# Performance work log

Measured on AMD Instinct MI355X. Metric: run time of the kernel, lower is better.

Reference implementation:

```python
import jax, jax.numpy as jnp
import numpy as np

EPS = 1e-5  # BatchNorm eps (torch default)

def setup_inputs() -> dict:
    key = jax.random.key(0)
    ks = jax.random.split(key, 24)
    B, NX, NY, F = 8, 128, 128, 128
    dims = [2 * F, 512, 256, 128, 64]
    d = {
        'x': jax.random.normal(ks[0], (B, NX, F), dtype=jnp.float32),
        'y': jax.random.normal(ks[1], (B, NY, F), dtype=jnp.float32),
    }
    i = 2
    for li, (din, dout) in enumerate(zip(dims[:-1], dims[1:]), start=1):
        d[f'w{li}'] = jax.random.normal(ks[i], (dout, din), dtype=jnp.float32) * (1.0 / np.sqrt(din)); i += 1
        d[f'b{li}'] = jax.random.normal(ks[i], (dout,), dtype=jnp.float32) * 0.02; i += 1
        if li < 4:  # BatchNorm1d on hidden layers only (eval mode: running stats)
            d[f'g{li}'] = 1.0 + 0.1 * jax.random.normal(ks[i], (dout,), dtype=jnp.float32); i += 1
            d[f'be{li}'] = 0.1 * jax.random.normal(ks[i], (dout,), dtype=jnp.float32); i += 1
            d[f'm{li}'] = 0.1 * jax.random.normal(ks[i], (dout,), dtype=jnp.float32); i += 1
            d[f'v{li}'] = 0.5 + jax.random.uniform(ks[i], (dout,), dtype=jnp.float32); i += 1
    return d

def _bn(h, g, be, m, v):
    # BatchNorm1d in eval mode over the channel (last) axis
    return (h - m) * (g * jax.lax.rsqrt(v + EPS)) + be

def reference(x, y,
              w1, b1, g1, be1, m1, v1,
              w2, b2, g2, be2, m2, v2,
              w3, b3, g3, be3, m3, v3,
              w4, b4):
    F = x.shape[-1]
    # First Linear on cat([x_i, y_j]) == split-weight broadcast add: avoids the
    # (B,nx,ny,2F) pairwise concat the torch code materializes (same math).
    wx, wy = w1[:, :F], w1[:, F:]                      # (512,F) each
    hx = jnp.einsum('bif,hf->bih', x, wx)              # (B,nx,512)
    hy = jnp.einsum('bjf,hf->bjh', y, wy)              # (B,ny,512)
    h = hx[:, :, None, :] + hy[:, None, :, :] + b1     # (B,nx,ny,512)
    h = jax.nn.relu(_bn(h, g1, be1, m1, v1))           # dropout is identity in eval
    h = jax.nn.relu(_bn(jnp.einsum('bijh,oh->bijo', h, w2) + b2, g2, be2, m2, v2))
    h = jax.nn.relu(_bn(jnp.einsum('bijh,oh->bijo', h, w3) + b3, g3, be3, m3, v3))
    e = jnp.einsum('bijh,oh->bijo', h, w4) + b4        # (B,nx,ny,64) embeddings
    # PSD path: einsum('bijk,bilk->bijl', e, e).sum(-1)
    #         == sum_k e[b,i,j,k] * (sum_l e[b,i,l,k])  -- avoids (B,nx,ny,ny)
    s = e.sum(axis=2)                                  # (B,nx,64)
    kernel = jnp.einsum('bijk,bik->bij', e, s)         # (B,nx,ny)
    return kernel
```

## Files before the change

### kernel.cpp

```cpp
#include <hip/hip_runtime.h>

#define EPS 1e-5f

typedef _Float16 half8 __attribute__((ext_vector_type(8)));
typedef _Float16 half4 __attribute__((ext_vector_type(4)));
typedef float f32x16 __attribute__((ext_vector_type(16)));
typedef float f32x4v __attribute__((ext_vector_type(4)));


__global__ __launch_bounds__(256)
void pre_kernel(
    const float* __restrict__ x, const float* __restrict__ y,
    const float* __restrict__ w1, const float* __restrict__ b1,
    const float* __restrict__ g1, const float* __restrict__ be1,
    const float* __restrict__ m1, const float* __restrict__ v1,
    const float* __restrict__ w2, const float* __restrict__ b2,
    const float* __restrict__ g2, const float* __restrict__ be2,
    const float* __restrict__ m2, const float* __restrict__ v2,
    const float* __restrict__ w3, const float* __restrict__ b3,
    const float* __restrict__ g3, const float* __restrict__ be3,
    const float* __restrict__ m3, const float* __restrict__ v3,
    const float* __restrict__ w4,
    _Float16* __restrict__ hxh, _Float16* __restrict__ hyh,
    _Float16* __restrict__ w2h, _Float16* __restrict__ w3h,
    _Float16* __restrict__ w4h,
    float* __restrict__ b2f, float* __restrict__ b3f)
{
    const int t = threadIdx.x;

    if (blockIdx.x >= 256) {
        int tid = (blockIdx.x - 256) * 256 + t;
        const int nth = 64 * 256;
        for (int idx = tid; idx < 256 * 512; idx += nth) {
            int n = idx >> 9, k = idx & 511;
            float a = g2[n] * rsqrtf(v2[n] + EPS);
            int addr = ((n >> 5) * 32 + (k >> 4)) * 512 + ((k >> 3) & 1) * 256 + (n & 31) * 8 + (k & 7);
            w2h[addr] = (_Float16)(a * w2[idx]);
        }
        for (int idx = tid; idx < 128 * 256; idx += nth) {
            int n = idx >> 8, k = idx & 255;
            float a = g3[n] * rsqrtf(v3[n] + EPS);
            int addr = ((n >> 5) * 16 + (k >> 4)) * 512 + ((k >> 3) & 1) * 256 + (n & 31) * 8 + (k & 7);
            w3h[addr] = (_Float16)(a * w3[idx]);
        }
        for (int idx = tid; idx < 64 * 128; idx += nth) {
            int n = idx >> 7, k = idx & 127;
            int addr = ((n >> 5) * 8 + (k >> 4)) * 512 + ((k >> 3) & 1) * 256 + (n & 31) * 8 + (k & 7);
            w4h[addr] = (_Float16)w4[idx];
        }
        if (tid < 256) {
            float a = g2[tid] * rsqrtf(v2[tid] + EPS);
            b2f[tid] = a * b2[tid] + be2[tid] - m2[tid] * a;
        } else if (tid < 384) {
            int n = tid - 256;
            float a = g3[n] * rsqrtf(v3[n] + EPS);
            b3f[n] = a * b3[n] + be3[n] - m3[n] * a;
        }
        return;
    }

    const int rg = blockIdx.x & 31;
    const int ng = (blockIdx.x >> 5) & 3;
    const int which = blockIdx.x >> 7;

    constexpr int LDA = 136;
    __shared__ _Float16 sh[32 * 136 + 128 * 136] __attribute__((aligned(16)));
    _Float16* xa = sh;
    _Float16* wb = sh + 32 * 136;

    const int rowbase = rg * 32;
    const float* src = which ? y : x;

#pragma unroll
    for (int p = 0; p < 4; ++p) {
        int c = p * 256 + t;
        int r = c >> 5, fo = (c & 31) * 4;
        f32x4v v = *(const f32x4v*)(src + (size_t)(rowbase + r) * 128 + fo);
        half4 h; h[0] = (_Float16)v[0]; h[1] = (_Float16)v[1];
        h[2] = (_Float16)v[2]; h[3] = (_Float16)v[3];
        *(half4*)(xa + r * LDA + fo) = h;
    }
#pragma unroll
    for (int p = 0; p < 16; ++p) {
        int c = p * 256 + t;
        int n = c >> 5, fo = (c & 31) * 4;
        f32x4v v = *(const f32x4v*)(w1 + (size_t)(ng * 128 + n) * 256 + which * 128 + fo);
        half4 h; h[0] = (_Float16)v[0]; h[1] = (_Float16)v[1];
        h[2] = (_Float16)v[2]; h[3] = (_Float16)v[3];
        *(half4*)(wb + n * LDA + fo) = h;
    }
    __syncthreads();

    const int wid = t >> 6;
    const int l = t & 63;
    const int l31 = l & 31, lh = l >> 5;

    f32x16 acc = (f32x16)0.f;
#pragma unroll
    for (int kc = 0; kc < 8; ++kc) {
        half8 af = *(const half8*)(xa + l31 * LDA + kc * 16 + lh * 8);
        half8 bf = *(const half8*)(wb + (wid * 32 + l31) * LDA + kc * 16 + lh * 8);
        acc = __builtin_amdgcn_mfma_f32_32x32x16_f16(af, bf, acc, 0, 0, 0);
    }

    const int n = ng * 128 + wid * 32 + l31;
    float alpha = g1[n] * rsqrtf(v1[n] + EPS);
    if (which == 0) {
        float bias = alpha * b1[n] + be1[n] - m1[n] * alpha;
#pragma unroll
        for (int r = 0; r < 16; ++r) {
            int m = (r & 3) + 8 * (r >> 2) + 4 * lh;
            hxh[(size_t)(rowbase + m) * 512 + n] = (_Float16)(alpha * acc[r] + bias);
        }
    } else {
        const int ks = n >> 4, lhh = (n >> 3) & 1, c = n & 7;
#pragma unroll
        for (int r = 0; r < 16; ++r) {
            int m = (r & 3) + 8 * (r >> 2) + 4 * lh;
            int R = rowbase + m;
            int bb = R >> 7, j = R & 127;
            int addr = bb * 65536 + ((j >> 5) * 32 + ks) * 512 + lhh * 256 + (j & 31) * 8 + c;
            hyh[addr] = (_Float16)(alpha * acc[r]);
        }
    }
}

__global__ __launch_bounds__(512, 2)
void fused_kernel(
    const _Float16* __restrict__ hxh, const _Float16* __restrict__ hyh,
    const _Float16* __restrict__ w2h, const _Float16* __restrict__ w3h,
    const _Float16* __restrict__ w4h,
    const float* __restrict__ b2f, const float* __restrict__ b3f,
    const float* __restrict__ b4,
    float* __restrict__ out)
{
    constexpr int LD2 = 264;
    constexpr int LD3 = 136;
    constexpr int LDE = 68;

    __shared__ char smem[4352 + 67584] __attribute__((aligned(16)));
    _Float16* hxs = (_Float16*)smem;
    float* spart  = (float*)(smem + 2048);
    float* ss     = (float*)(smem + 4096);
    char* R1 = smem + 4352;
    _Float16* a2  = (_Float16*)R1;
    _Float16* a3  = (_Float16*)R1;
    float*    es  = (float*)R1;

    const int b  = blockIdx.x >> 6;
    const int ip = blockIdx.x & 63;
    const int i0 = ip * 2;
    const int t = threadIdx.x;
    const int wid = t >> 6;
    const int l   = t & 63;
    const int l31 = l & 31;
    const int lh  = l >> 5;

    if (t < 128) {
        int iv = t >> 6;
        *(half8*)(hxs + iv * 512 + (t & 63) * 8) =
            *(const half8*)(hxh + (size_t)(b * 128 + i0 + iv) * 512 + (t & 63) * 8);
    }
    __syncthreads();

    const int wm = wid >> 2, wn = wid & 3;

    const _Float16* pa0 = hyh + (size_t)b * 65536 + (size_t)(2 * wm) * 32 * 512 + l * 8;
    const _Float16* pa1 = pa0 + 32 * 512;
    const _Float16* pb0 = w2h + (size_t)(2 * wn) * 32 * 512 + l * 8;
    const _Float16* pb1 = pb0 + 32 * 512;

    const float bb0 = b2f[wn * 64 + l31];
    const float bb1 = b2f[wn * 64 + 32 + l31];
    f32x16 d00 = (f32x16)bb0, d01 = (f32x16)bb1;
    f32x16 d10 = (f32x16)bb0, d11 = (f32x16)bb1;
    f32x16 e00 = (f32x16)bb0, e01 = (f32x16)bb1;
    f32x16 e10 = (f32x16)bb0, e11 = (f32x16)bb1;

    half8 A00, A01, B00, B01;
    half8 A10, A11, B10, B11;

    auto LD0 = [&](int ks) {
        A00 = *(const half8*)(pa0 + (size_t)ks * 512);
        A01 = *(const half8*)(pa1 + (size_t)ks * 512);
        B00 = *(const half8*)(pb0 + (size_t)ks * 512);
        B01 = *(const half8*)(pb1 + (size_t)ks * 512);
    };
    auto LD1 = [&](int ks) {
        A10 = *(const half8*)(pa0 + (size_t)ks * 512);
        A11 = *(const half8*)(pa1 + (size_t)ks * 512);
        B10 = *(const half8*)(pb0 + (size_t)ks * 512);
        B11 = *(const half8*)(pb1 + (size_t)ks * 512);
    };
    auto RELU = [&](half8 a, half8 rx) {
        half8 s = a + rx;
        half8 af;
#pragma unroll
        for (int c = 0; c < 8; ++c)
            af[c] = s[c] > (_Float16)0.f ? s[c] : (_Float16)0.f;
        return af;
    };
    auto STEP0 = [&](int ks) {
        half8 rx0 = *(const half8*)(hxs + ks * 16 + lh * 8);
        half8 rx1 = *(const half8*)(hxs + 512 + ks * 16 + lh * 8);
        half8 af;
        af = RELU(A00, rx0);
        d00 = __builtin_amdgcn_mfma_f32_32x32x16_f16(af, B00, d00, 0, 0, 0);
        d01 = __builtin_amdgcn_mfma_f32_32x32x16_f16(af, B01, d01, 0, 0, 0);
        af = RELU(A01, rx0);
        d10 = __builtin_amdgcn_mfma_f32_32x32x16_f16(af, B00, d10, 0, 0, 0);
        d11 = __builtin_amdgcn_mfma_f32_32x32x16_f16(af, B01, d11, 0, 0, 0);
        af = RELU(A00, rx1);
        e00 = __builtin_amdgcn_mfma_f32_32x32x16_f16(af, B00, e00, 0, 0, 0);
        e01 = __builtin_amdgcn_mfma_f32_32x32x16_f16(af, B01, e01, 0, 0, 0);
        af = RELU(A01, rx1);
        e10 = __builtin_amdgcn_mfma_f32_32x32x16_f16(af, B00, e10, 0, 0, 0);
        e11 = __builtin_amdgcn_mfma_f32_32x32x16_f16(af, B01, e11, 0, 0, 0);
    };
    auto STEP1 = [&](int ks) {
        half8 rx0 = *(const half8*)(hxs + ks * 16 + lh * 8);
        half8 rx1 = *(const half8*)(hxs + 512 + ks * 16 + lh * 8);
        half8 af;
        af = RELU(A10, rx0);
        d00 = __builtin_amdgcn_mfma_f32_32x32x16_f16(af, B10, d00, 0, 0, 0);
        d01 = __builtin_amdgcn_mfma_f32_32x32x16_f16(af, B11, d01, 0, 0, 0);
        af = RELU(A11, rx0);
        d10 = __builtin_amdgcn_mfma_f32_32x32x16_f16(af, B10, d10, 0, 0, 0);
        d11 = __builtin_amdgcn_mfma_f32_32x32x16_f16(af, B11, d11, 0, 0, 0);
        af = RELU(A10, rx1);
        e00 = __builtin_amdgcn_mfma_f32_32x32x16_f16(af, B10, e00, 0, 0, 0);
        e01 = __builtin_amdgcn_mfma_f32_32x32x16_f16(af, B11, e01, 0, 0, 0);
        af = RELU(A11, rx1);
        e10 = __builtin_amdgcn_mfma_f32_32x32x16_f16(af, B10, e10, 0, 0, 0);
        e11 = __builtin_amdgcn_mfma_f32_32x32x16_f16(af, B11, e11, 0, 0, 0);
    };

    LD0(0);
#pragma unroll 2
    for (int ks = 0; ks < 32; ks += 2) {
        if (ks + 1 < 32) LD1(ks + 1);
        STEP0(ks);
        if (ks + 2 < 32) LD0(ks + 2);
        if (ks + 1 < 32) STEP1(ks + 1);
    }

    auto TAIL = [&](const f32x16& a00, const f32x16& a01,
                    const f32x16& a10, const f32x16& a11, int iv) {
#pragma unroll
        for (int r = 0; r < 16; ++r) {
            int m = wm * 64 + (r & 3) + 8 * (r >> 2) + 4 * lh;
            a2[m * LD2 + wn * 64 + l31]               = (_Float16)fmaxf(a00[r], 0.f);
            a2[m * LD2 + wn * 64 + 32 + l31]          = (_Float16)fmaxf(a01[r], 0.f);
            a2[(m + 32) * LD2 + wn * 64 + l31]        = (_Float16)fmaxf(a10[r], 0.f);
            a2[(m + 32) * LD2 + wn * 64 + 32 + l31]   = (_Float16)fmaxf(a11[r], 0.f);
        }
        __syncthreads();

        f32x16 g0, g1;
        {
            float b3v = b3f[wn * 32 + l31];
            g0 = (f32x16)b3v;
            g1 = (f32x16)b3v;
        }
#pragma unroll 4
        for (int kc = 0; kc < 16; ++kc) {
            half8 bfr = *(const half8*)(w3h + (wn * 16 + kc) * 512 + l * 8);
            half8 af0 = *(const half8*)(a2 + (wm * 64 + l31) * LD2 + kc * 16 + lh * 8);
            half8 af1 = *(const half8*)(a2 + (wm * 64 + 32 + l31) * LD2 + kc * 16 + lh * 8);
            g0 = __builtin_amdgcn_mfma_f32_32x32x16_f16(af0, bfr, g0, 0, 0, 0);
            g1 = __builtin_amdgcn_mfma_f32_32x32x16_f16(af1, bfr, g1, 0, 0, 0);
        }
        __syncthreads();
#pragma unroll
        for (int mt = 0; mt < 2; ++mt)
#pragma unroll
            for (int r = 0; r < 16; ++r) {
                int m = wm * 64 + mt * 32 + (r & 3) + 8 * (r >> 2) + 4 * lh;
                a3[m * LD3 + wn * 32 + l31] = (_Float16)fmaxf(mt ? g1[r] : g0[r], 0.f);
            }
        __syncthreads();

        const int wm4 = wid >> 1, wn4 = wid & 1;
        f32x16 acc4 = (f32x16)(b4[wn4 * 32 + l31]);
#pragma unroll
        for (int kc = 0; kc < 8; ++kc) {
            half8 afr = *(const half8*)(a3 + (wm4 * 32 + l31) * LD3 + kc * 16 + lh * 8);
            half8 bfr = *(const half8*)(w4h + (wn4 * 8 + kc) * 512 + l * 8);
            acc4 = __builtin_amdgcn_mfma_f32_32x32x16_f16(afr, bfr, acc4, 0, 0, 0);
        }
        __syncthreads();
#pragma unroll
        for (int r = 0; r < 16; ++r) {
            int m = wm4 * 32 + (r & 3) + 8 * (r >> 2) + 4 * lh;
            es[m * LDE + wn4 * 32 + l31] = acc4[r];
        }
        __syncthreads();

        {
            float sv = 0.f;
#pragma unroll
            for (int jj = 0; jj < 16; ++jj) sv += es[(wid + jj * 8) * LDE + l];
            spart[wid * 64 + l] = sv;
        }
        __syncthreads();
        if (t < 64) {
            float s2 = 0.f;
#pragma unroll
            for (int r = 0; r < 8; ++r) s2 += spart[r * 64 + t];
            ss[t] = s2;
        }
        __syncthreads();
        {
            const int j = t >> 2, q = t & 3;
            float p = 0.f;
#pragma unroll
            for (int c = 0; c < 16; ++c) {
                int k = q + 4 * c;
                p += es[j * LDE + k] * ss[k];
            }
            p += __shfl_xor(p, 1);
            p += __shfl_xor(p, 2);
            if (q == 0) out[(size_t)(b * 128 + iv) * 128 + j] = p;
        }
        __syncthreads();
    };

    TAIL(d00, d01, d10, d11, i0);
    TAIL(e00, e01, e10, e11, i0 + 1);
}

extern "C" void kernel_launch(void* const* d_in, const int* in_sizes, int n_in,
                              void* d_out, int out_size, void* d_ws, size_t ws_size,
                              hipStream_t stream)
{
    (void)in_sizes; (void)n_in; (void)out_size; (void)ws_size;

    const float* x   = (const float*)d_in[0];
    const float* y   = (const float*)d_in[1];
    const float* w1  = (const float*)d_in[2];
    const float* b1  = (const float*)d_in[3];
    const float* g1  = (const float*)d_in[4];
    const float* be1 = (const float*)d_in[5];
    const float* m1  = (const float*)d_in[6];
    const float* v1  = (const float*)d_in[7];
    const float* w2  = (const float*)d_in[8];
    const float* b2  = (const float*)d_in[9];
    const float* g2  = (const float*)d_in[10];
    const float* be2 = (const float*)d_in[11];
    const float* m2  = (const float*)d_in[12];
    const float* v2  = (const float*)d_in[13];
    const float* w3  = (const float*)d_in[14];
    const float* b3  = (const float*)d_in[15];
    const float* g3  = (const float*)d_in[16];
    const float* be3 = (const float*)d_in[17];
    const float* m3  = (const float*)d_in[18];
    const float* v3  = (const float*)d_in[19];
    const float* w4  = (const float*)d_in[20];
    const float* b4  = (const float*)d_in[21];
    float* out = (float*)d_out;

    float* b2f = (float*)d_ws;
    float* b3f = b2f + 256;
    _Float16* w2h = (_Float16*)(b3f + 128);
    _Float16* w3h = w2h + 131072;
    _Float16* w4h = w3h + 32768;
    _Float16* hxh = w4h + 8192;
    _Float16* hyh = hxh + 524288;

    hipLaunchKernelGGL(pre_kernel, dim3(320), dim3(256), 0, stream,
                       x, y, w1, b1, g1, be1, m1, v1,
                       w2, b2, g2, be2, m2, v2,
                       w3, b3, g3, be3, m3, v3,
                       w4,
                       hxh, hyh, w2h, w3h, w4h, b2f, b3f);

    hipLaunchKernelGGL(fused_kernel, dim3(512), dim3(512), 0, stream,
                       hxh, hyh, w2h, w3h, w4h, b2f, b3f, b4, out);
}
```

Measured before the change: 67.21 us.

## Double fused kernel block to 1024 threads with smaller per-wave tiles

Result: slower. 73.29 us (+9.0%).

```diff
diff --git a/kernel.cpp b/kernel.cpp
--- a/kernel.cpp
+++ b/kernel.cpp
@@ -125,7 +125,7 @@
     }
 }
 
-__global__ __launch_bounds__(512, 2)
+__global__ __launch_bounds__(1024, 4)
 void fused_kernel(
     const _Float16* __restrict__ hxh, const _Float16* __restrict__ hyh,
     const _Float16* __restrict__ w2h, const _Float16* __restrict__ w3h,
@@ -138,11 +138,11 @@
     constexpr int LD3 = 136;
     constexpr int LDE = 68;
 
-    __shared__ char smem[4352 + 67584] __attribute__((aligned(16)));
+    __shared__ char smem[6400 + 67584] __attribute__((aligned(16)));
     _Float16* hxs = (_Float16*)smem;
     float* spart  = (float*)(smem + 2048);
-    float* ss     = (float*)(smem + 4096);
-    char* R1 = smem + 4352;
+    float* ss     = (float*)(smem + 6144);
+    char* R1 = smem + 6400;
     _Float16* a2  = (_Float16*)R1;
     _Float16* a3  = (_Float16*)R1;
     float*    es  = (float*)R1;
@@ -165,30 +165,25 @@
 
     const int wm = wid >> 2, wn = wid & 3;
 
-    const _Float16* pa0 = hyh + (size_t)b * 65536 + (size_t)(2 * wm) * 32 * 512 + l * 8;
-    const _Float16* pa1 = pa0 + 32 * 512;
+    const _Float16* pa  = hyh + (size_t)b * 65536 + (size_t)(wm * 32) * 512 + l * 8;
     const _Float16* pb0 = w2h + (size_t)(2 * wn) * 32 * 512 + l * 8;
     const _Float16* pb1 = pb0 + 32 * 512;
 
     const float bb0 = b2f[wn * 64 + l31];
     const float bb1 = b2f[wn * 64 + 32 + l31];
-    f32x16 d00 = (f32x16)bb0, d01 = (f32x16)bb1;
-    f32x16 d10 = (f32x16)bb0, d11 = (f32x16)bb1;
-    f32x16 e00 = (f32x16)bb0, e01 = (f32x16)bb1;
-    f32x16 e10 = (f32x16)bb0, e11 = (f32x16)bb1;
-
-    half8 A00, A01, B00, B01;
-    half8 A10, A11, B10, B11;
+    f32x16 d0 = (f32x16)bb0, d1 = (f32x16)bb1;
+    f32x16 e0 = (f32x16)bb0, e1 = (f32x16)bb1;
+
+    half8 A0, B00, B01;
+    half8 A1, B10, B11;
 
     auto LD0 = [&](int ks) {
-        A00 = *(const half8*)(pa0 + (size_t)ks * 512);
-        A01 = *(const half8*)(pa1 + (size_t)ks * 512);
+        A0  = *(const half8*)(pa  + (size_t)ks * 512);
         B00 = *(const half8*)(pb0 + (size_t)ks * 512);
         B01 = *(const half8*)(pb1 + (size_t)ks * 512);
     };
     auto LD1 = [&](int ks) {
-        A10 = *(const half8*)(pa0 + (size_t)ks * 512);
-        A11 = *(const half8*)(pa1 + (size_t)ks * 512);
+        A1  = *(const half8*)(pa  + (size_t)ks * 512);
         B10 = *(const half8*)(pb0 + (size_t)ks * 512);
         B11 = *(const half8*)(pb1 + (size_t)ks * 512);
     };
@@ -203,36 +198,22 @@
     auto STEP0 = [&](int ks) {
         half8 rx0 = *(const half8*)(hxs + ks * 16 + lh * 8);
         half8 rx1 = *(const half8*)(hxs + 512 + ks * 16 + lh * 8);
-        half8 af;
-        af = RELU(A00, rx0);
-        d00 = __builtin_amdgcn_mfma_f32_32x32x16_f16(af, B00, d00, 0, 0, 0);
-        d01 = __builtin_amdgcn_mfma_f32_32x32x16_f16(af, B01, d01, 0, 0, 0);
-        af = RELU(A01, rx0);
-        d10 = __builtin_amdgcn_mfma_f32_32x32x16_f16(af, B00, d10, 0, 0, 0);
-        d11 = __builtin_amdgcn_mfma_f32_32x32x16_f16(af, B01, d11, 0, 0, 0);
-        af = RELU(A00, rx1);
-        e00 = __builtin_amdgcn_mfma_f32_32x32x16_f16(af, B00, e00, 0, 0, 0);
-        e01 = __builtin_amdgcn_mfma_f32_32x32x16_f16(af, B01, e01, 0, 0, 0);
-        af = RELU(A01, rx1);
-        e10 = __builtin_amdgcn_mfma_f32_32x32x16_f16(af, B00, e10, 0, 0, 0);
-        e11 = __builtin_amdgcn_mfma_f32_32x32x16_f16(af, B01, e11, 0, 0, 0);
+        half8 af = RELU(A0, rx0);
+        d0 = __builtin_amdgcn_mfma_f32_32x32x16_f16(af, B00, d0, 0, 0, 0);
+        d1 = __builtin_amdgcn_mfma_f32_32x32x16_f16(af, B01, d1, 0, 0, 0);
+        af = RELU(A0, rx1);
+        e0 = __builtin_amdgcn_mfma_f32_32x32x16_f16(af, B00, e0, 0, 0, 0);
+        e1 = __builtin_amdgcn_mfma_f32_32x32x16_f16(af, B01, e1, 0, 0, 0);
     };
     auto STEP1 = [&](int ks) {
         half8 rx0 = *(const half8*)(hxs + ks * 16 + lh * 8);
         half8 rx1 = *(const half8*)(hxs + 512 + ks * 16 + lh * 8);
-        half8 af;
-        af = RELU(A10, rx0);
-        d00 = __builtin_amdgcn_mfma_f32_32x32x16_f16(af, B10, d00, 0, 0, 0);
-        d01 = __builtin_amdgcn_mfma_f32_32x32x16_f16(af, B11, d01, 0, 0, 0);
-        af = RELU(A11, rx0);
-        d10 = __builtin_amdgcn_mfma_f32_32x32x16_f16(af, B10, d10, 0, 0, 0);
-        d11 = __builtin_amdgcn_mfma_f32_32x32x16_f16(af, B11, d11, 0, 0, 0);
-        af = RELU(A10, rx1);
-        e00 = __builtin_amdgcn_mfma_f32_32x32x16_f16(af, B10, e00, 0, 0, 0);
-        e01 = __builtin_amdgcn_mfma_f32_32x32x16_f16(af, B11, e01, 0, 0, 0);
-        af = RELU(A11, rx1);
-        e10 = __builtin_amdgcn_mfma_f32_32x32x16_f16(af, B10, e10, 0, 0, 0);
-        e11 = __builtin_amdgcn_mfma_f32_32x32x16_f16(af, B11, e11, 0, 0, 0);
+        half8 af = RELU(A1, rx0);
+        d0 = __builtin_amdgcn_mfma_f32_32x32x16_f16(af, B10, d0, 0, 0, 0);
+        d1 = __builtin_amdgcn_mfma_f32_32x32x16_f16(af, B11, d1, 0, 0, 0);
+        af = RELU(A1, rx1);
+        e0 = __builtin_amdgcn_mfma_f32_32x32x16_f16(af, B10, e0, 0, 0, 0);
+        e1 = __builtin_amdgcn_mfma_f32_32x32x16_f16(af, B11, e1, 0, 0, 0);
     };
 
     LD0(0);
@@ -244,89 +225,83 @@
         if (ks + 1 < 32) STEP1(ks + 1);
     }
 
-    auto TAIL = [&](const f32x16& a00, const f32x16& a01,
-                    const f32x16& a10, const f32x16& a11, int iv) {
+    auto TAIL = [&](const f32x16& c0, const f32x16& c1, int iv) {
 #pragma unroll
         for (int r = 0; r < 16; ++r) {
-            int m = wm * 64 + (r & 3) + 8 * (r >> 2) + 4 * lh;
-            a2[m * LD2 + wn * 64 + l31]               = (_Float16)fmaxf(a00[r], 0.f);
-            a2[m * LD2 + wn * 64 + 32 + l31]          = (_Float16)fmaxf(a01[r], 0.f);
-            a2[(m + 32) * LD2 + wn * 64 + l31]        = (_Float16)fmaxf(a10[r], 0.f);
-            a2[(m + 32) * LD2 + wn * 64 + 32 + l31]   = (_Float16)fmaxf(a11[r], 0.f);
-        }
-        __syncthreads();
-
-        f32x16 g0, g1;
-        {
-            float b3v = b3f[wn * 32 + l31];
-            g0 = (f32x16)b3v;
-            g1 = (f32x16)b3v;
-        }
+            int m = wm * 32 + (r & 3) + 8 * (r >> 2) + 4 * lh;
+            a2[m * LD2 + wn * 64 + l31]      = (_Float16)fmaxf(c0[r], 0.f);
+            a2[m * LD2 + wn * 64 + 32 + l31] = (_Float16)fmaxf(c1[r], 0.f);
+        }
+        __syncthreads();
+
+        f32x16 g = (f32x16)(b3f[wn * 32 + l31]);
 #pragma unroll 4
         for (int kc = 0; kc < 16; ++kc) {
             half8 bfr = *(const half8*)(w3h + (wn * 16 + kc) * 512 + l * 8);
-            half8 af0 = *(const half8*)(a2 + (wm * 64 + l31) * LD2 + kc * 16 + lh * 8);
-            half8 af1 = *(const half8*)(a2 + (wm * 64 + 32 + l31) * LD2 + kc * 16 + lh * 8);
-            g0 = __builtin_amdgcn_mfma_f32_32x32x16_f16(af0, bfr, g0, 0, 0, 0);
-            g1 = __builtin_amdgcn_mfma_f32_32x32x16_f16(af1, bfr, g1, 0, 0, 0);
-        }
-        __syncthreads();
-#pragma unroll
-        for (int mt = 0; mt < 2; ++mt)
+            half8 af  = *(const half8*)(a2 + (wm * 32 + l31) * LD2 + kc * 16 + lh * 8);
+            g = __builtin_amdgcn_mfma_f32_32x32x16_f16(af, bfr, g, 0, 0, 0);
+        }
+        __syncthreads();
+#pragma unroll
+        for (int r = 0; r < 16; ++r) {
+            int m = wm * 32 + (r & 3) + 8 * (r >> 2) + 4 * lh;
+            a3[m * LD3 + wn * 32 + l31] = (_Float16)fmaxf(g[r], 0.f);
+        }
+        __syncthreads();
+
+        f32x16 acc4;
+        const int wm4 = wid >> 1, wn4 = wid & 1;
+        if (wid < 8) {
+            acc4 = (f32x16)(b4[wn4 * 32 + l31]);
+#pragma unroll
+            for (int kc = 0; kc < 8; ++kc) {
+                half8 afr = *(const half8*)(a3 + (wm4 * 32 + l31) * LD3 + kc * 16 + lh * 8);
+                half8 bfr = *(const half8*)(w4h + (wn4 * 8 + kc) * 512 + l * 8);
+                acc4 = __builtin_amdgcn_mfma_f32_32x32x16_f16(afr, bfr, acc4, 0, 0, 0);
+            }
+        }
+        __syncthreads();
+        if (wid < 8) {
 #pragma unroll
             for (int r = 0; r < 16; ++r) {
-                int m = wm * 64 + mt * 32 + (r & 3) + 8 * (r >> 2) + 4 * lh;
-                a3[m * LD3 + wn * 32 + l31] = (_Float16)fmaxf(mt ? g1[r] : g0[r], 0.f);
+                int m = wm4 * 32 + (r & 3) + 8 * (r >> 2) + 4 * lh;
+                es[m * LDE + wn4 * 32 + l31] = acc4[r];
             }
-        __syncthreads();
-
-        const int wm4 = wid >> 1, wn4 = wid & 1;
-        f32x16 acc4 = (f32x16)(b4[wn4 * 32 + l31]);
-#pragma unroll
-        for (int kc = 0; kc < 8; ++kc) {
-            half8 afr = *(const half8*)(a3 + (wm4 * 32 + l31) * LD3 + kc * 16 + lh * 8);
-            half8 bfr = *(const half8*)(w4h + (wn4 * 8 + kc) * 512 + l * 8);
-            acc4 = __builtin_amdgcn_mfma_f32_32x32x16_f16(afr, bfr, acc4, 0, 0, 0);
-        }
-        __syncthreads();
-#pragma unroll
-        for (int r = 0; r < 16; ++r) {
-            int m = wm4 * 32 + (r & 3) + 8 * (r >> 2) + 4 * lh;
-            es[m * LDE + wn4 * 32 + l31] = acc4[r];
         }
         __syncthreads();
 
         {
             float sv = 0.f;
 #pragma unroll
-            for (int jj = 0; jj < 16; ++jj) sv += es[(wid + jj * 8) * LDE + l];
+            for (int jj = 0; jj < 8; ++jj) sv += es[(wid + jj * 16) * LDE + l];
             spart[wid * 64 + l] = sv;
         }
         __syncthreads();
         if (t < 64) {
             float s2 = 0.f;
 #pragma unroll
-            for (int r = 0; r < 8; ++r) s2 += spart[r * 64 + t];
+            for (int r = 0; r < 16; ++r) s2 += spart[r * 64 + t];
             ss[t] = s2;
         }
         __syncthreads();
         {
-            const int j = t >> 2, q = t & 3;
+            const int j = t >> 3, q = t & 7;
             float p = 0.f;
 #pragma unroll
-            for (int c = 0; c < 16; ++c) {
-                int k = q + 4 * c;
+            for (int c = 0; c < 8; ++c) {
+                int k = q + 8 * c;
                 p += es[j * LDE + k] * ss[k];
             }
             p += __shfl_xor(p, 1);
             p += __shfl_xor(p, 2);
+            p += __shfl_xor(p, 4);
             if (q == 0) out[(size_t)(b * 128 + iv) * 128 + j] = p;
         }
         __syncthreads();
     };
 
-    TAIL(d00, d01, d10, d11, i0);
-    TAIL(e00, e01, e10, e11, i0 + 1);
+    TAIL(d0, d1, i0);
+    TAIL(e0, e1, i0 + 1);
 }
 
 extern "C" void kernel_launch(void* const* d_in, const int* in_sizes, int n_in,
@@ -374,6 +349,6 @@
                        w4,
                        hxh, hyh, w2h, w3h, w4h, b2f, b3f);
 
-    hipLaunchKernelGGL(fused_kernel, dim3(512), dim3(512), 0, stream,
+    hipLaunchKernelGGL(fused_kernel, dim3(512), dim3(1024), 0, stream,
                        hxh, hyh, w2h, w3h, w4h, b2f, b3f, b4, out);
 }
```
